# Kernel optimization log

Hardware: AMD Instinct MI355X
Metric: run time of the kernel (lower is better)

## Reference

```python
import jax, jax.numpy as jnp
import numpy as np

BIN_SIZE = 256  # init arg bin_size
K = 16          # init arg k


def setup_inputs() -> dict:
    key = jax.random.key(0)
    k1, k2 = jax.random.split(key)
    x = jax.random.normal(k1, (2, 8192, 256), dtype=jnp.float32)          # (B, N, D)
    codebook = jax.random.normal(k2, (256, 32), dtype=jnp.float32)        # (D, max_num_bins//2)
    return {"x": x, "codebook": codebook}


def reference(x, codebook):
    B, N, D = x.shape
    n_bins = N // BIN_SIZE
    # LSH binning: project onto random hyperplanes, argmax over [proj, -proj]
    mul = jnp.matmul(x, codebook[:, : n_bins // 2])          # (B, N, n_bins//2)
    cmul = jnp.concatenate([mul, -mul], axis=-1)             # (B, N, n_bins)
    bin_idx = jnp.argmax(cmul, axis=-1)                      # (B, N)
    # stable sort points by bin id -> equal-size bins (matches torch.argsort)
    bins_split = jnp.argsort(bin_idx, axis=-1).reshape(B, n_bins, BIN_SIZE)
    # gather points into bins
    pts = jnp.take_along_axis(x, bins_split.reshape(B, N, 1), axis=1)
    pts = pts.reshape(B, n_bins, BIN_SIZE, D)
    # per-bin dense similarity + sigmoid
    dm = jax.nn.sigmoid(jnp.einsum('bnid,bnjd->bnik'.replace('k', 'j'), pts, pts))  # (B, n_bins, BIN, BIN)
    vals, inds = jax.lax.top_k(dm, K)                        # (B, n_bins, BIN, K)
    # map local bin indices back to global point indices
    flat_split = bins_split.reshape(B, N)
    bin_off = jnp.arange(n_bins, dtype=inds.dtype)[None, :, None, None] * BIN_SIZE
    gdst = jnp.take_along_axis(flat_split, (bin_off + inds).reshape(B, -1), axis=1)
    gdst = gdst.reshape(B, n_bins, BIN_SIZE, K)
    gsrc = jnp.broadcast_to(bins_split[..., None], vals.shape)
    bidx = jnp.broadcast_to(jnp.arange(B)[:, None, None, None], vals.shape)
    # coalesced sparse adjacency, represented densely (duplicates summed like coalesce())
    out = jnp.zeros((B, N, N), x.dtype).at[bidx, gsrc, gdst].add(vals)
    return out
```

## Files before the change

### kernel.cpp

```cpp
#include <hip/hip_runtime.h>
#include <math.h>

#define BB    2
#define NN    8192
#define DD    256
#define NBINS 32
#define BINSZ 256
#define NPROJ 16
#define TOPK  16
#define NPTS  (BB * NN)

typedef float vf4 __attribute__((ext_vector_type(4)));

__global__ __launch_bounds__(64) void k_bins(const float* __restrict__ x,
                                             const float* __restrict__ cb,
                                             int* __restrict__ bin_idx) {
    __shared__ double cbd[DD][NPROJ];
    const int t = threadIdx.x;
    for (int q = t; q < DD * 4; q += 64) {
        int d = q >> 2, j4 = q & 3;
        float4 v = *(const float4*)(cb + d * 32 + j4 * 4);
        cbd[d][j4 * 4 + 0] = (double)v.x;
        cbd[d][j4 * 4 + 1] = (double)v.y;
        cbd[d][j4 * 4 + 2] = (double)v.z;
        cbd[d][j4 * 4 + 3] = (double)v.w;
    }
    __syncthreads();

    const int p = blockIdx.x * 64 + t;
    const float* xr = x + (size_t)p * DD;

    double a[NPROJ];
#pragma unroll
    for (int j = 0; j < NPROJ; ++j) a[j] = 0.0;

    for (int d0 = 0; d0 < DD; d0 += 4) {
        float4 xv = *(const float4*)(xr + d0);
        float xs[4] = {xv.x, xv.y, xv.z, xv.w};
#pragma unroll
        for (int dd = 0; dd < 4; ++dd) {
            double xd = (double)xs[dd];
#pragma unroll
            for (int j = 0; j < NPROJ; ++j)
                a[j] = fma(cbd[d0 + dd][j], xd, a[j]);
        }
    }

    float bv = -INFINITY; int bj = 0;
#pragma unroll
    for (int j = 0; j < NPROJ; ++j) {
        float m = (float)a[j];
        if (m > bv) { bv = m; bj = j; }
    }
#pragma unroll
    for (int j = 0; j < NPROJ; ++j) {
        float m = -(float)a[j];
        if (m > bv) { bv = m; bj = j + NPROJ; }
    }
    bin_idx[p] = bj;
}

__global__ __launch_bounds__(256) void k_sort(const int* __restrict__ bin_idx,
                                              int* __restrict__ order) {
    __shared__ int c[NBINS][256];
    __shared__ int base[NBINS];
    const int t = threadIdx.x;
    const int b = blockIdx.x;
    const int* bi = bin_idx + b * NN;

    for (int j = 0; j < NBINS; ++j) c[j][t] = 0;
    __syncthreads();

    const int i0 = t * 32;
    for (int i = 0; i < 32; ++i) c[bi[i0 + i]][t]++;
    __syncthreads();

    if (t < NBINS) {
        int s = 0;
        for (int q = 0; q < 256; ++q) s += c[t][q];
        base[t] = s;
    }
    __syncthreads();
    if (t == 0) {
        int run = 0;
        for (int j = 0; j < NBINS; ++j) { int tmp = base[j]; base[j] = run; run += tmp; }
    }
    __syncthreads();
    if (t < NBINS) {
        int run = base[t];
        for (int q = 0; q < 256; ++q) { int tmp = c[t][q]; c[t][q] = run; run += tmp; }
    }
    __syncthreads();

    int* ob = order + b * NN;
    for (int i = 0; i < 32; ++i) {
        int gi = i0 + i;
        int bb = bi[gi];
        int pos = c[bb][t]++;
        ob[pos] = gi;
    }
}

#define RT 32
__global__ __launch_bounds__(256, 2) void k_sim(const float* __restrict__ x,
                                                const int* __restrict__ order,
                                                float* __restrict__ out) {
    __shared__ int   idx[BINSZ];
    __shared__ float Bt[BINSZ][36];
    __shared__ float S[RT][BINSZ + 1];
    __shared__ float tvs[RT][TOPK];
    __shared__ int   tds[RT][TOPK];

    const int t   = threadIdx.x;
    const int bid = blockIdx.x;
    const int b   = bid >> 8;
    const int bin = (bid >> 3) & 31;
    const int r0  = (bid & 7) * RT;

    idx[t] = order[b * NN + bin * BINSZ + t];
    __syncthreads();

    const float* xb = x + (size_t)b * NN * DD;

    const int sr_ = t >> 3, sc = t & 7;
    const float* srow[8];
#pragma unroll
    for (int q = 0; q < 8; ++q)
        srow[q] = xb + (size_t)idx[sr_ + 32 * q] * DD + sc * 4;

    const int rg    = t >> 6;
    const int cbase = t & 63;

    double acc[8][4];
#pragma unroll
    for (int r = 0; r < 8; ++r)
#pragma unroll
        for (int k = 0; k < 4; ++k) acc[r][k] = 0.0;

    const vf4 z4 = (vf4)0.0f;

#pragma unroll 1
    for (int it = 0; it < 8; ++it) {
        const int k0 = it * 32;

        float4 st[8];
#pragma unroll
        for (int q = 0; q < 8; ++q) st[q] = *(const float4*)(srow[q] + k0);

        {
            const int zr = it * 4;
#pragma unroll
            for (int rr = 0; rr < 4; ++rr) {
                vf4* orow = (vf4*)(out + ((size_t)b * NN + idx[r0 + zr + rr]) * NN);
#pragma unroll
                for (int j = 0; j < 8; ++j)
                    __builtin_nontemporal_store(z4, orow + j * 256 + t);
            }
        }

        __syncthreads();
#pragma unroll
        for (int q = 0; q < 8; ++q)
            *(float4*)&Bt[sr_ + 32 * q][sc * 4] = st[q];
        __syncthreads();

#pragma unroll
        for (int dd4 = 0; dd4 < 8; ++dd4) {
            float4 af[8];
#pragma unroll
            for (int rr = 0; rr < 8; ++rr)
                af[rr] = *(const float4*)&Bt[r0 + rg * 8 + rr][dd4 * 4];
            float4 bf[4];
#pragma unroll
            for (int k = 0; k < 4; ++k)
                bf[k] = *(const float4*)&Bt[cbase + 64 * k][dd4 * 4];

#pragma unroll
            for (int e = 0; e < 4; ++e) {
                float ae[8], be[4];
#pragma unroll
                for (int rr = 0; rr < 8; ++rr)
                    ae[rr] = (e == 0) ? af[rr].x : (e == 1) ? af[rr].y
                           : (e == 2) ? af[rr].z : af[rr].w;
#pragma unroll
                for (int k = 0; k < 4; ++k)
                    be[k] = (e == 0) ? bf[k].x : (e == 1) ? bf[k].y
                          : (e == 2) ? bf[k].z : bf[k].w;
                double ad[8], bd[4];
#pragma unroll
                for (int rr = 0; rr < 8; ++rr) ad[rr] = (double)ae[rr];
#pragma unroll
                for (int k = 0; k < 4; ++k)    bd[k]  = (double)be[k];
#pragma unroll
                for (int rr = 0; rr < 8; ++rr)
#pragma unroll
                    for (int k = 0; k < 4; ++k)
                        acc[rr][k] = fma(ad[rr], bd[k], acc[rr][k]);
            }
        }
    }

#pragma unroll
    for (int rr = 0; rr < 8; ++rr)
#pragma unroll
        for (int k = 0; k < 4; ++k) {
            float s32 = (float)acc[rr][k];
            S[rg * 8 + rr][cbase + 64 * k] = 1.0f / (1.0f + expf(-s32));
        }
    __syncthreads();

    if (t < RT) {
        float tv[TOPK]; int ti[TOPK];
#pragma unroll
        for (int q = 0; q < TOPK; ++q) { tv[q] = -INFINITY; ti[q] = 0; }
        for (int cc = 0; cc < BINSZ; ++cc) {
            float v = S[t][cc];
            if (v > tv[TOPK - 1]) {
                tv[TOPK - 1] = v; ti[TOPK - 1] = cc;
#pragma unroll
                for (int q = TOPK - 1; q > 0; --q) {
                    if (tv[q] > tv[q - 1]) {
                        float fv = tv[q]; tv[q] = tv[q - 1]; tv[q - 1] = fv;
                        int   fi = ti[q]; ti[q] = ti[q - 1]; ti[q - 1] = fi;
                    }
                }
            }
        }
#pragma unroll
        for (int q = 0; q < TOPK; ++q) {
            tvs[t][q] = tv[q];
            tds[t][q] = idx[ti[q]];
        }
    }
    __syncthreads();

#pragma unroll
    for (int p = t; p < RT * TOPK; p += 256) {
        int r = p >> 4, q = p & 15;
        float* orow = out + ((size_t)b * NN + idx[r0 + r]) * NN;
        orow[tds[r][q]] = tvs[r][q];
    }
}

extern "C" void kernel_launch(void* const* d_in, const int* in_sizes, int n_in,
                              void* d_out, int out_size, void* d_ws, size_t ws_size,
                              hipStream_t stream) {
    const float* x  = (const float*)d_in[0];
    const float* cb = (const float*)d_in[1];
    float* out      = (float*)d_out;

    int* bin_idx = (int*)d_ws;
    int* order   = bin_idx + NPTS;

    k_bins<<<NPTS / 64, 64, 0, stream>>>(x, cb, bin_idx);
    k_sort<<<BB, 256, 0, stream>>>(bin_idx, order);
    k_sim<<<BB * NBINS * 8, 256, 0, stream>>>(x, order, out);
}
```

Baseline: 696.5 us.

## Stage only row tile in LDS and stream column operands from global registers

Before, each iteration of the k_sim loop staged a 256x32 slice of the gathered bin in shared memory, with two barriers per step. Now only the block's 32 row vectors (full depth) are loaded into LDS once up front. Each thread reads its 4 column points straight from global memory into registers, 16 dims per step, which removes the per-iteration barriers and LDS stores. The trade-off is more global/L2 traffic, since column rows are reloaded per thread and across the 8 row-blocks of each bin, plus higher register pressure from the bv array. Zero-fill stores are spread over 16 iterations of 2 rows instead of 8 iterations of 4.

```diff
diff --git a/kernel.cpp b/kernel.cpp
--- a/kernel.cpp
+++ b/kernel.cpp
@@ -106,7 +106,7 @@
                                                 const int* __restrict__ order,
                                                 float* __restrict__ out) {
     __shared__ int   idx[BINSZ];
-    __shared__ float Bt[BINSZ][36];
+    __shared__ float As[RT][260];
     __shared__ float S[RT][BINSZ + 1];
     __shared__ float tvs[RT][TOPK];
     __shared__ int   tds[RT][TOPK];
@@ -122,14 +122,23 @@
 
     const float* xb = x + (size_t)b * NN * DD;
 
-    const int sr_ = t >> 3, sc = t & 7;
-    const float* srow[8];
-#pragma unroll
-    for (int q = 0; q < 8; ++q)
-        srow[q] = xb + (size_t)idx[sr_ + 32 * q] * DD + sc * 4;
+    {
+        const int ar = t >> 3;
+        const int ac = t & 7;
+        const float* ag = xb + (size_t)idx[r0 + ar] * DD;
+#pragma unroll
+        for (int q = 0; q < 8; ++q) {
+            float4 v = *(const float4*)(ag + (ac + 8 * q) * 4);
+            *(float4*)&As[ar][(ac + 8 * q) * 4] = v;
+        }
+    }
 
     const int rg    = t >> 6;
     const int cbase = t & 63;
+    const float* colp[4];
+#pragma unroll
+    for (int k = 0; k < 4; ++k)
+        colp[k] = xb + (size_t)idx[cbase + 64 * k] * DD;
 
     double acc[8][4];
 #pragma unroll
@@ -139,18 +148,23 @@
 
     const vf4 z4 = (vf4)0.0f;
 
+    __syncthreads();
+
 #pragma unroll 1
-    for (int it = 0; it < 8; ++it) {
-        const int k0 = it * 32;
-
-        float4 st[8];
-#pragma unroll
-        for (int q = 0; q < 8; ++q) st[q] = *(const float4*)(srow[q] + k0);
+    for (int it = 0; it < 16; ++it) {
+        const int k0 = it * 16;
+
+        float4 bv[4][4];
+#pragma unroll
+        for (int k = 0; k < 4; ++k)
+#pragma unroll
+            for (int q = 0; q < 4; ++q)
+                bv[k][q] = *(const float4*)(colp[k] + k0 + q * 4);
 
         {
-            const int zr = it * 4;
-#pragma unroll
-            for (int rr = 0; rr < 4; ++rr) {
+            const int zr = it * 2;
+#pragma unroll
+            for (int rr = 0; rr < 2; ++rr) {
                 vf4* orow = (vf4*)(out + ((size_t)b * NN + idx[r0 + zr + rr]) * NN);
 #pragma unroll
                 for (int j = 0; j < 8; ++j)
@@ -158,44 +172,30 @@
             }
         }
 
-        __syncthreads();
-#pragma unroll
-        for (int q = 0; q < 8; ++q)
-            *(float4*)&Bt[sr_ + 32 * q][sc * 4] = st[q];
-        __syncthreads();
-
-#pragma unroll
-        for (int dd4 = 0; dd4 < 8; ++dd4) {
+#pragma unroll
+        for (int dd4 = 0; dd4 < 4; ++dd4) {
             float4 af[8];
 #pragma unroll
             for (int rr = 0; rr < 8; ++rr)
-                af[rr] = *(const float4*)&Bt[r0 + rg * 8 + rr][dd4 * 4];
-            float4 bf[4];
-#pragma unroll
-            for (int k = 0; k < 4; ++k)
-                bf[k] = *(const float4*)&Bt[cbase + 64 * k][dd4 * 4];
-
+                af[rr] = *(const float4*)&As[rg * 8 + rr][k0 + dd4 * 4];
+            const float4 b0 = bv[0][dd4], b1 = bv[1][dd4],
+                         b2 = bv[2][dd4], b3 = bv[3][dd4];
 #pragma unroll
             for (int e = 0; e < 4; ++e) {
-                float ae[8], be[4];
-#pragma unroll
-                for (int rr = 0; rr < 8; ++rr)
-                    ae[rr] = (e == 0) ? af[rr].x : (e == 1) ? af[rr].y
-                           : (e == 2) ? af[rr].z : af[rr].w;
-#pragma unroll
-                for (int k = 0; k < 4; ++k)
-                    be[k] = (e == 0) ? bf[k].x : (e == 1) ? bf[k].y
-                          : (e == 2) ? bf[k].z : bf[k].w;
-                double ad[8], bd[4];
-#pragma unroll
-                for (int rr = 0; rr < 8; ++rr) ad[rr] = (double)ae[rr];
-#pragma unroll
-                for (int k = 0; k < 4; ++k)    bd[k]  = (double)be[k];
-#pragma unroll
-                for (int rr = 0; rr < 8; ++rr)
-#pragma unroll
-                    for (int k = 0; k < 4; ++k)
-                        acc[rr][k] = fma(ad[rr], bd[k], acc[rr][k]);
+                const double be0 = (double)((e == 0) ? b0.x : (e == 1) ? b0.y : (e == 2) ? b0.z : b0.w);
+                const double be1 = (double)((e == 0) ? b1.x : (e == 1) ? b1.y : (e == 2) ? b1.z : b1.w);
+                const double be2 = (double)((e == 0) ? b2.x : (e == 1) ? b2.y : (e == 2) ? b2.z : b2.w);
+                const double be3 = (double)((e == 0) ? b3.x : (e == 1) ? b3.y : (e == 2) ? b3.z : b3.w);
+#pragma unroll
+                for (int rr = 0; rr < 8; ++rr) {
+                    const float ae = (e == 0) ? af[rr].x : (e == 1) ? af[rr].y
+                                   : (e == 2) ? af[rr].z : af[rr].w;
+                    const double ad = (double)ae;
+                    acc[rr][0] = fma(ad, be0, acc[rr][0]);
+                    acc[rr][1] = fma(ad, be1, acc[rr][1]);
+                    acc[rr][2] = fma(ad, be2, acc[rr][2]);
+                    acc[rr][3] = fma(ad, be3, acc[rr][3]);
+                }
             }
         }
     }
```

Result: faster. 661.7 us (-5.0%).
